# Kernel optimization log

Measured on AMD Instinct MI355X. Metric: run time of the kernel, lower is better.

The kernel has to match this reference:

```python
import math
import jax, jax.numpy as jnp
import numpy as np

L, D, H, DF, V, T, B = 4, 1024, 16, 4096, 32000, 2048, 1
HD = D // H
EPS = 1e-5

def _ln(x, w, b):
    m = jnp.mean(x, -1, keepdims=True)
    v = jnp.mean((x - m) ** 2, -1, keepdims=True)
    return (x - m) * jax.lax.rsqrt(v + EPS) * w + b

def setup_inputs() -> dict:
    key = jax.random.key(0)
    ks = jax.random.split(key, 8)
    s = 0.02
    return {
        'ids':   jax.random.randint(ks[0], (B, T), 0, V),
        'te':    jax.random.normal(ks[1], (V, D), jnp.float32) * s,
        'pe':    jax.random.normal(ks[2], (T, D), jnp.float32) * s,
        'qkv_w': jax.random.normal(ks[3], (L, D, 3 * D), jnp.float32) * s,
        'qkv_b': jnp.zeros((L, 3 * D), jnp.float32),
        'out_w': jax.random.normal(ks[4], (L, D, D), jnp.float32) * s,
        'out_b': jnp.zeros((L, D), jnp.float32),
        'ln1_w': jnp.ones((L, D), jnp.float32),
        'ln1_b': jnp.zeros((L, D), jnp.float32),
        'ln2_w': jnp.ones((L, D), jnp.float32),
        'ln2_b': jnp.zeros((L, D), jnp.float32),
        'up_w':  jax.random.normal(ks[5], (L, D, DF), jnp.float32) * s,
        'up_b':  jnp.zeros((L, DF), jnp.float32),
        'dn_w':  jax.random.normal(ks[6], (L, DF, D), jnp.float32) * s,
        'dn_b':  jnp.zeros((L, D), jnp.float32),
        'lnf_w': jnp.ones((D,), jnp.float32),
        'lnf_b': jnp.zeros((D,), jnp.float32),
    }

def reference(ids, te, pe, qkv_w, qkv_b, out_w, out_b, ln1_w, ln1_b,
              ln2_w, ln2_b, up_w, up_b, dn_w, dn_b, lnf_w, lnf_b):
    b, t = ids.shape
    x = te[ids] + pe[:t][None]                        # [b,t,D]
    causal = jnp.tril(jnp.ones((t, t), bool))          # [t,t]
    scale = 1.0 / math.sqrt(HD)
    for i in range(L):
        h = _ln(x, ln1_w[i], ln1_b[i])
        qkv = (h @ qkv_w[i] + qkv_b[i]).reshape(b, t, 3, H, HD)
        q, k, v = qkv[:, :, 0], qkv[:, :, 1], qkv[:, :, 2]
        sc = jnp.einsum('bqhd,bkhd->bhqk', q, k) * scale
        sc = jnp.where(causal, sc, -jnp.inf)
        att = jax.nn.softmax(sc, axis=-1)
        ao = jnp.einsum('bhqk,bkhd->bqhd', att, v).reshape(b, t, D)
        x = x + ao @ out_w[i] + out_b[i]
        h = _ln(x, ln2_w[i], ln2_b[i])
        x = x + jax.nn.silu(h @ up_w[i] + up_b[i]) @ dn_w[i] + dn_b[i]
    x = _ln(x, lnf_w, lnf_b)
    logits = x @ te.T                                  # tied head, no bias
    return logits
```

## Files before the change

kernel.cpp:

```cpp
#include <hip/hip_runtime.h>

typedef __attribute__((ext_vector_type(8))) short short8;
typedef __attribute__((ext_vector_type(4))) short short4v;
typedef __attribute__((ext_vector_type(4))) float f32x4;
typedef unsigned short u16;

#define Lc 4
#define Dc 1024
#define Hc 16
#define HDc 64
#define DFc 4096
#define Vc 32000
#define Tc 2048

__device__ __forceinline__ u16 f2bf(float f) {
  union { float f; unsigned u; } v; v.f = f;
  return (u16)((v.u + 0x7FFFu + ((v.u >> 16) & 1u)) >> 16);
}

__device__ __forceinline__ void gload_lds16(const u16* g, u16* l) {
  __builtin_amdgcn_global_load_lds(
      (const __attribute__((address_space(1))) unsigned int*)(g),
      (__attribute__((address_space(3))) unsigned int*)(l), 16, 0, 0);
}

#define BARS do { __builtin_amdgcn_s_barrier(); __builtin_amdgcn_sched_barrier(0); } while (0)
#define LGKM0 do { asm volatile("s_waitcnt lgkmcnt(0)" ::: "memory"); __builtin_amdgcn_sched_barrier(0); } while (0)
#define VMC(n) do { asm volatile("s_waitcnt vmcnt(" #n ")" ::: "memory"); __builtin_amdgcn_sched_barrier(0); } while (0)

__global__ __launch_bounds__(256) void castk(const float* __restrict__ in, u16* __restrict__ out) {
  size_t i = ((size_t)blockIdx.x * 256 + threadIdx.x) * 4;
  float4 v = *(const float4*)(in + i);
  short4v o; o[0] = f2bf(v.x); o[1] = f2bf(v.y); o[2] = f2bf(v.z); o[3] = f2bf(v.w);
  *(short4v*)(out + i) = o;
}

__global__ __launch_bounds__(256) void embedln(const int* __restrict__ ids, const float* __restrict__ te,
                                               const float* __restrict__ pe, const float* __restrict__ w,
                                               const float* __restrict__ b, float* __restrict__ x,
                                               u16* __restrict__ out) {
  int t = blockIdx.x, tid = threadIdx.x;
  int id = ids[t];
  float4 a = *(const float4*)(te + (size_t)id * Dc + tid * 4);
  float4 p = *(const float4*)(pe + (size_t)t * Dc + tid * 4);
  float4 v; v.x = a.x + p.x; v.y = a.y + p.y; v.z = a.z + p.z; v.w = a.w + p.w;
  size_t i = (size_t)t * Dc + tid * 4;
  *(float4*)(x + i) = v;
  float s = v.x + v.y + v.z + v.w;
  float q = v.x * v.x + v.y * v.y + v.z * v.z + v.w * v.w;
  #pragma unroll
  for (int off = 1; off < 64; off <<= 1) { s += __shfl_xor(s, off); q += __shfl_xor(q, off); }
  __shared__ float red[8];
  if ((tid & 63) == 0) { red[tid >> 6] = s; red[4 + (tid >> 6)] = q; }
  __syncthreads();
  s = red[0] + red[1] + red[2] + red[3];
  q = red[4] + red[5] + red[6] + red[7];
  float mean = s * (1.0f / Dc);
  float rstd = rsqrtf(q * (1.0f / Dc) - mean * mean + 1e-5f);
  float4 wv = *(const float4*)(w + tid * 4);
  float4 bv = *(const float4*)(b + tid * 4);
  out[i + 0] = f2bf((v.x - mean) * rstd * wv.x + bv.x);
  out[i + 1] = f2bf((v.y - mean) * rstd * wv.y + bv.y);
  out[i + 2] = f2bf((v.z - mean) * rstd * wv.z + bv.z);
  out[i + 3] = f2bf((v.w - mean) * rstd * wv.w + bv.w);
}

template<int SK>
__global__ __launch_bounds__(256) void combineln(float* __restrict__ x, const float* __restrict__ p,
                                                 const float* __restrict__ bias, const float* __restrict__ w,
                                                 const float* __restrict__ b, u16* __restrict__ out) {
  int t = blockIdx.x, tid = threadIdx.x;
  size_t i = (size_t)t * Dc + tid * 4;
  float4 v = *(const float4*)(x + i);
  #pragma unroll
  for (int s = 0; s < SK; s++) {
    float4 q2 = *(const float4*)(p + (size_t)s * Tc * Dc + i);
    v.x += q2.x; v.y += q2.y; v.z += q2.z; v.w += q2.w;
  }
  float4 bb = *(const float4*)(bias + tid * 4);
  v.x += bb.x; v.y += bb.y; v.z += bb.z; v.w += bb.w;
  *(float4*)(x + i) = v;
  float s = v.x + v.y + v.z + v.w;
  float q = v.x * v.x + v.y * v.y + v.z * v.z + v.w * v.w;
  #pragma unroll
  for (int off = 1; off < 64; off <<= 1) { s += __shfl_xor(s, off); q += __shfl_xor(q, off); }
  __shared__ float red[8];
  if ((tid & 63) == 0) { red[tid >> 6] = s; red[4 + (tid >> 6)] = q; }
  __syncthreads();
  s = red[0] + red[1] + red[2] + red[3];
  q = red[4] + red[5] + red[6] + red[7];
  float mean = s * (1.0f / Dc);
  float rstd = rsqrtf(q * (1.0f / Dc) - mean * mean + 1e-5f);
  float4 wv = *(const float4*)(w + tid * 4);
  float4 bv = *(const float4*)(b + tid * 4);
  out[i + 0] = f2bf((v.x - mean) * rstd * wv.x + bv.x);
  out[i + 1] = f2bf((v.y - mean) * rstd * wv.y + bv.y);
  out[i + 2] = f2bf((v.z - mean) * rstd * wv.z + bv.z);
  out[i + 3] = f2bf((v.w - mean) * rstd * wv.w + bv.w);
}

__global__ __launch_bounds__(256) void transpose4(const float* __restrict__ qw, const float* __restrict__ ow,
                                                  const float* __restrict__ uw, const float* __restrict__ dw,
                                                  u16* __restrict__ qT, u16* __restrict__ oT,
                                                  u16* __restrict__ uT, u16* __restrict__ dT) {
  __shared__ float tl[32][33];
  int id = blockIdx.x;
  const float* in; u16* out; int R, C, t;
  if (id < 3072)      { in = qw; out = qT; R = Dc;  C = 3 * Dc; t = id; }
  else if (id < 4096) { in = ow; out = oT; R = Dc;  C = Dc;     t = id - 3072; }
  else if (id < 8192) { in = uw; out = uT; R = Dc;  C = DFc;    t = id - 4096; }
  else                { in = dw; out = dT; R = DFc; C = Dc;     t = id - 8192; }
  int tilesX = C >> 5;
  int c0 = (t % tilesX) * 32, r0 = (t / tilesX) * 32;
  int lx = threadIdx.x & 31, ly = threadIdx.x >> 5;
  #pragma unroll
  for (int i = ly; i < 32; i += 8) tl[i][lx] = in[(size_t)(r0 + i) * C + c0 + lx];
  __syncthreads();
  #pragma unroll
  for (int i = ly; i < 32; i += 8) out[(size_t)(c0 + i) * R + r0 + lx] = f2bf(tl[lx][i]);
}

template<int EPI>
__global__ __launch_bounds__(256) void gemm128m(
    const u16* __restrict__ A, const u16* __restrict__ Bt, const float* __restrict__ bias,
    u16* __restrict__ outb, float* __restrict__ outf, int M, int N, int K, int KS) {
  __shared__ __align__(16) u16 lds[32768];
  u16* As = lds;
  u16* Bs = lds + 16384;
  const int NK = KS >> 6;

  int tid = threadIdx.x;
  int w = tid >> 6, lane = tid & 63;
  int lr = lane & 15, lg = lane >> 4;
  int wr = w >> 1, wc = w & 1;

  int m0 = blockIdx.y * 128, n0 = blockIdx.x * 128;
  int kbase = blockIdx.z * KS;

  int offg[4];
  #pragma unroll
  for (int j = 0; j < 4; j++) {
    int p = tid + j * 256;
    int row = p >> 3;
    int uc = (p & 7) ^ (row & 7);
    offg[j] = row * K + uc * 8;
  }
  const u16* aB = A + (size_t)m0 * K + kbase;
  const u16* bB = Bt + (size_t)n0 * K + kbase;

  auto stA = [&](int kt) {
    u16* l = As + ((kt & 1) << 13) + w * 512;
    #pragma unroll
    for (int j = 0; j < 4; j++)
      gload_lds16(aB + kt * 64 + offg[j], l + j * 2048);
  };
  auto stB = [&](int kt) {
    u16* l = Bs + ((kt & 1) << 13) + w * 512;
    #pragma unroll
    for (int j = 0; j < 4; j++)
      gload_lds16(bB + kt * 64 + offg[j], l + j * 2048);
  };

  int colx0 = ((0 * 4 + lg) ^ (lr & 7)) * 8;
  int colx1 = ((1 * 4 + lg) ^ (lr & 7)) * 8;
  int abase = (wr * 64 + lr) * 64;
  int bbase = (wc * 64 + lr) * 64;

  f32x4 acc[4][4] = {};

  stB(0); stA(0); stB(1);
  VMC(4);
  BARS;

  for (int kt = 0; kt < NK; ++kt) {
    const u16* sA = As + ((kt & 1) << 13);
    const u16* sB = Bs + ((kt & 1) << 13);
    short8 af[4][2], bf[4][2];

    #pragma unroll
    for (int m = 0; m < 2; m++) {
      af[m][0] = *(const short8*)(sA + abase + m * 1024 + colx0);
      af[m][1] = *(const short8*)(sA + abase + m * 1024 + colx1);
    }
    #pragma unroll
    for (int n = 0; n < 4; n++) {
      bf[n][0] = *(const short8*)(sB + bbase + n * 1024 + colx0);
      bf[n][1] = *(const short8*)(sB + bbase + n * 1024 + colx1);
    }
    if (kt + 1 < NK) stA(kt + 1);
    BARS;
    LGKM0;
    __builtin_amdgcn_s_setprio(1);
    #pragma unroll
    for (int m = 0; m < 2; m++)
      #pragma unroll
      for (int n = 0; n < 4; n++)
        #pragma unroll
        for (int ks = 0; ks < 2; ks++)
          acc[m][n] = __builtin_amdgcn_mfma_f32_16x16x32_bf16(af[m][ks], bf[n][ks], acc[m][n], 0, 0, 0);
    __builtin_amdgcn_s_setprio(0);
    BARS;

    #pragma unroll
    for (int m = 2; m < 4; m++) {
      af[m][0] = *(const short8*)(sA + abase + m * 1024 + colx0);
      af[m][1] = *(const short8*)(sA + abase + m * 1024 + colx1);
    }
    if (kt + 2 < NK) { stB(kt + 2); VMC(4); }
    else if (kt + 1 < NK) { VMC(0); }
    BARS;
    LGKM0;
    __builtin_amdgcn_s_setprio(1);
    #pragma unroll
    for (int m = 2; m < 4; m++)
      #pragma unroll
      for (int n = 0; n < 4; n++)
        #pragma unroll
        for (int ks = 0; ks < 2; ks++)
          acc[m][n] = __builtin_amdgcn_mfma_f32_16x16x32_bf16(af[m][ks], bf[n][ks], acc[m][n], 0, 0, 0);
    __builtin_amdgcn_s_setprio(0);
    BARS;
  }

  if (EPI == 0 || EPI == 1 || (EPI == 5 && n0 < 2 * Dc)) {
    u16* lu = lds;
    BARS;
    #pragma unroll
    for (int n = 0; n < 4; n++) {
      int col = wc * 64 + n * 16 + lr;
      float bv = bias[n0 + col];
      #pragma unroll
      for (int m = 0; m < 4; m++) {
        #pragma unroll
        for (int r = 0; r < 4; r++) {
          int rl = wr * 64 + m * 16 + lg * 4 + r;
          float v = acc[m][n][r] + bv;
          if (EPI == 1) v = v / (1.0f + __expf(-v));
          lu[rl * 128 + (col ^ (((rl >> 2) & 3) << 4))] = f2bf(v);
        }
      }
    }
    BARS;
    #pragma unroll
    for (int j = 0; j < 8; j++) {
      int i8 = j * 2048 + tid * 8;
      int row = i8 >> 7;
      int col8 = i8 & 127;
      short8 v = *(const short8*)(lu + row * 128 + (col8 ^ (((row >> 2) & 3) << 4)));
      *(short8*)(outb + (size_t)(m0 + row) * N + n0 + col8) = v;
    }
  } else if (EPI == 4) {
    float* lf = (float*)lds;
    float* op = outf + (size_t)blockIdx.z * M * N;
    #pragma unroll
    for (int pass = 0; pass < 2; pass++) {
      BARS;
      if (wr == pass) {
        #pragma unroll
        for (int n = 0; n < 4; n++) {
          int col = wc * 64 + n * 16 + lr;
          #pragma unroll
          for (int m = 0; m < 4; m++)
            #pragma unroll
            for (int r = 0; r < 4; r++) {
              int rl = m * 16 + lg * 4 + r;
              lf[rl * 128 + (col ^ (((rl >> 2) & 1) << 4))] = acc[m][n][r];
            }
        }
      }
      BARS;
      #pragma unroll
      for (int j = 0; j < 8; j++) {
        int i4 = j * 1024 + tid * 4;
        int row = i4 >> 7;
        int col4 = i4 & 127;
        f32x4 v = *(const f32x4*)(lf + row * 128 + (col4 ^ (((row >> 2) & 1) << 4)));
        *(f32x4*)(op + (size_t)(m0 + pass * 64 + row) * N + n0 + col4) = v;
      }
    }
  } else {
    u16* vtp = (u16*)outf;
    #pragma unroll
    for (int n = 0; n < 4; n++) {
      int gn = n0 + wc * 64 + n * 16 + lr;
      float bv = bias[gn];
      #pragma unroll
      for (int m = 0; m < 4; m++) {
        int gmb = m0 + wr * 64 + m * 16 + lg * 4;
        short4v o;
        #pragma unroll
        for (int r = 0; r < 4; r++) o[r] = (short)f2bf(acc[m][n][r] + bv);
        *(short4v*)(vtp + (size_t)(gn - 2 * Dc) * Tc + gmb) = o;
      }
    }
  }
}

__global__ __launch_bounds__(512) void gemm256(const u16* __restrict__ A, const u16* __restrict__ Bt,
                                               float* __restrict__ outf, int M, int N, int K) {
  __shared__ __align__(16) u16 lds[65536];
  u16* AsU = lds;
  u16* BsU = lds + 32768;
  const int NK = K >> 6;

  int tid = threadIdx.x;
  int w = tid >> 6, lane = tid & 63;
  int lr = lane & 15, lg = lane >> 4;
  int wr = w >> 2, wc = w & 3;

  int flat = blockIdx.y * gridDim.x + blockIdx.x;
  {
    int nwg = gridDim.x * gridDim.y;
    int q = nwg >> 3, r = nwg & 7, xc = flat & 7, s = flat >> 3;
    flat = (xc < r ? xc * (q + 1) : r * (q + 1) + (xc - r) * q) + s;
  }
  int bm = flat % gridDim.x, bn = flat / gridDim.x;
  int m0 = bm * 256, n0 = bn * 256;

  int row0 = tid >> 3;
  int uc0 = (tid & 7) ^ (row0 & 7);
  int offg = row0 * K + uc0 * 8;
  const u16* aB = A + (size_t)m0 * K;
  const u16* bB = Bt + (size_t)n0 * K;

  auto stA = [&](int kt, int half) {
    const u16* g = aB + (size_t)half * 128 * K + kt * 64 + offg;
    u16* l = AsU + (((kt & 1) * 2 + half) << 13) + w * 512;
    gload_lds16(g, l);
    gload_lds16(g + 64 * K, l + 4096);
  };
  auto stB = [&](int kt, int half) {
    const u16* g = bB + (size_t)half * 128 * K + kt * 64 + offg;
    u16* l = BsU + (((kt & 1) * 2 + half) << 13) + w * 512;
    gload_lds16(g, l);
    gload_lds16(g + 64 * K, l + 4096);
  };

  int colx0 = ((0 * 4 + lg) ^ (lr & 7)) * 8;
  int colx1 = ((1 * 4 + lg) ^ (lr & 7)) * 8;
  int arow = lr * 64;
  int brow = ((wc & 1) * 64 + lr) * 64;

  f32x4 acc[8][4] = {};

  stB(0, 0); stB(0, 1); stA(0, 0); stA(0, 1); stB(1, 0); stB(1, 1);
  VMC(4);
  BARS;

  for (int kt = 0; kt < NK; ++kt) {
    int slot = kt & 1;
    const u16* sA = AsU + ((slot * 2 + wr) << 13);
    const u16* sB = BsU + ((slot * 2 + (wc >> 1)) << 13);
    short8 af0[4][2], af1[4][2], bf0[2][2], bf1[2][2];

    #pragma unroll
    for (int m = 0; m < 4; m++) {
      af0[m][0] = *(const short8*)(sA + arow + m * 1024 + colx0);
      af0[m][1] = *(const short8*)(sA + arow + m * 1024 + colx1);
    }
    #pragma unroll
    for (int n = 0; n < 2; n++) {
      bf0[n][0] = *(const short8*)(sB + brow + n * 1024 + colx0);
      bf0[n][1] = *(const short8*)(sB + brow + n * 1024 + colx1);
      bf1[n][0] = *(const short8*)(sB + brow + (n + 2) * 1024 + colx0);
      bf1[n][1] = *(const short8*)(sB + brow + (n + 2) * 1024 + colx1);
    }
    if (kt + 1 < NK) { stA(kt + 1, 0); stA(kt + 1, 1); }
    BARS;
    LGKM0;
    __builtin_amdgcn_s_setprio(1);
    #pragma unroll
    for (int m = 0; m < 4; m++)
      #pragma unroll
      for (int n = 0; n < 2; n++)
        #pragma unroll
        for (int ks = 0; ks < 2; ks++)
          acc[m][n] = __builtin_amdgcn_mfma_f32_16x16x32_bf16(af0[m][ks], bf0[n][ks], acc[m][n], 0, 0, 0);
    #pragma unroll
    for (int m = 0; m < 4; m++)
      #pragma unroll
      for (int n = 0; n < 2; n++)
        #pragma unroll
        for (int ks = 0; ks < 2; ks++)
          acc[m][n + 2] = __builtin_amdgcn_mfma_f32_16x16x32_bf16(af0[m][ks], bf1[n][ks], acc[m][n + 2], 0, 0, 0);
    __builtin_amdgcn_s_setprio(0);
    BARS;

    #pragma unroll
    for (int m = 0; m < 4; m++) {
      af1[m][0] = *(const short8*)(sA + arow + (m + 4) * 1024 + colx0);
      af1[m][1] = *(const short8*)(sA + arow + (m + 4) * 1024 + colx1);
    }
    if (kt + 2 < NK) { stB(kt + 2, 0); stB(kt + 2, 1); VMC(4); }
    else if (kt + 1 < NK) { VMC(0); }
    BARS;
    LGKM0;
    __builtin_amdgcn_s_setprio(1);
    #pragma unroll
    for (int m = 0; m < 4; m++)
      #pragma unroll
      for (int n = 0; n < 2; n++)
        #pragma unroll
        for (int ks = 0; ks < 2; ks++)
          acc[m + 4][n] = __builtin_amdgcn_mfma_f32_16x16x32_bf16(af1[m][ks], bf0[n][ks], acc[m + 4][n], 0, 0, 0);
    #pragma unroll
    for (int m = 0; m < 4; m++)
      #pragma unroll
      for (int n = 0; n < 2; n++)
        #pragma unroll
        for (int ks = 0; ks < 2; ks++)
          acc[m + 4][n + 2] = __builtin_amdgcn_mfma_f32_16x16x32_bf16(af1[m][ks], bf1[n][ks], acc[m + 4][n + 2], 0, 0, 0);
    __builtin_amdgcn_s_setprio(0);
    BARS;
  }

  {
    float* lf = (float*)lds;
    #pragma unroll
    for (int pass = 0; pass < 2; pass++) {
      BARS;
      if (wr == pass) {
        #pragma unroll
        for (int n = 0; n < 4; n++) {
          int col = wc * 64 + n * 16 + lr;
          #pragma unroll
          for (int m = 0; m < 8; m++)
            #pragma unroll
            for (int r = 0; r < 4; r++) {
              int rl = m * 16 + lg * 4 + r;
              lf[rl * 256 + (col ^ (((rl >> 2) & 1) << 4))] = acc[m][n][r];
            }
        }
      }
      BARS;
      #pragma unroll
      for (int j = 0; j < 16; j++) {
        int i4 = j * 2048 + tid * 4;
        int row = i4 >> 8;
        int col4 = i4 & 255;
        f32x4 v = *(const f32x4*)(lf + row * 256 + (col4 ^ (((row >> 2) & 1) << 4)));
        *(f32x4*)(outf + (size_t)(m0 + pass * 128 + row) * N + n0 + col4) = v;
      }
    }
  }
}

__global__ __launch_bounds__(512) void attnk(const u16* __restrict__ qkv, const u16* __restrict__ vt,
                                             u16* __restrict__ ao) {
  __shared__ u16 Plds[8][16][72];
  __shared__ float Cacc[4][64][16];
  __shared__ float Cl[4][64][4];
  int bid = blockIdx.x;
  int hh = bid >> 5;
  int qb = (bid & 256) ? (31 - (bid & 31)) : (bid & 31);
  int tid = threadIdx.x, l = tid & 63, w = tid >> 6;
  int w4 = w & 3, ishi = w >> 2;
  int lr = l & 15, lg = l >> 4;
  int qr0 = qb * 64 + w4 * 16;
  const u16* qbase = qkv + (size_t)(qr0 + lr) * (3 * Dc) + hh * HDc + lg * 8;
  short8 aq0 = *(const short8*)qbase;
  short8 aq1 = *(const short8*)(qbase + 32);
  f32x4 acco[4] = {};
  float rs[4] = {0.0f, 0.0f, 0.0f, 0.0f};
  int nkb = (qr0 + 79) >> 6;
  int half = nkb >> 1;
  int klo = ishi ? half : 0;
  int khi = ishi ? nkb : half;
  const float cl2 = 0.125f * 1.44269504088896f;
  for (int kb = klo; kb < khi; kb++) {
    int kk0 = kb * 64;
    float sv[4][4];
    bool msk = (kb == nkb - 1);
    #pragma unroll
    for (int st = 0; st < 4; st++) {
      int kt0 = kk0 + st * 16;
      const u16* kbase = qkv + (size_t)(kt0 + lr) * (3 * Dc) + Dc + hh * HDc + lg * 8;
      short8 bk0 = *(const short8*)kbase;
      short8 bk1 = *(const short8*)(kbase + 32);
      f32x4 s = {};
      s = __builtin_amdgcn_mfma_f32_16x16x32_bf16(aq0, bk0, s, 0, 0, 0);
      s = __builtin_amdgcn_mfma_f32_16x16x32_bf16(aq1, bk1, s, 0, 0, 0);
      if (msk) {
        int gcol = kt0 + lr;
        #pragma unroll
        for (int r = 0; r < 4; r++) {
          int grow = qr0 + lg * 4 + r;
          sv[st][r] = (gcol <= grow) ? s[r] * cl2 : -__builtin_inff();
        }
      } else {
        #pragma unroll
        for (int r = 0; r < 4; r++) sv[st][r] = s[r] * cl2;
      }
    }
    #pragma unroll
    for (int st = 0; st < 4; st++) {
      #pragma unroll
      for (int r = 0; r < 4; r++) {
        float p = __builtin_amdgcn_exp2f(fminf(sv[st][r], 45.0f));
        sv[st][r] = p;
        rs[r] += p;
      }
    }
    #pragma unroll
    for (int st = 0; st < 4; st++) {
      #pragma unroll
      for (int r = 0; r < 4; r++) Plds[w][lg * 4 + r][st * 16 + lr] = f2bf(sv[st][r]);
    }
    short8 pa0 = *(const short8*)&Plds[w][lr][lg * 8];
    short8 pa1 = *(const short8*)&Plds[w][lr][32 + lg * 8];
    #pragma unroll
    for (int nt = 0; nt < 4; nt++) {
      const u16* vbase = vt + (size_t)(hh * HDc + nt * 16 + lr) * Tc + kk0 + lg * 8;
      short8 bv0 = *(const short8*)vbase;
      short8 bv1 = *(const short8*)(vbase + 32);
      acco[nt] = __builtin_amdgcn_mfma_f32_16x16x32_bf16(pa0, bv0, acco[nt], 0, 0, 0);
      acco[nt] = __builtin_amdgcn_mfma_f32_16x16x32_bf16(pa1, bv1, acco[nt], 0, 0, 0);
    }
  }
  #pragma unroll
  for (int off = 1; off < 16; off <<= 1) {
    #pragma unroll
    for (int r = 0; r < 4; r++) rs[r] += __shfl_xor(rs[r], off);
  }
  if (ishi) {
    #pragma unroll
    for (int nt = 0; nt < 4; nt++)
      #pragma unroll
      for (int r = 0; r < 4; r++) Cacc[w4][l][nt * 4 + r] = acco[nt][r];
    #pragma unroll
    for (int r = 0; r < 4; r++) Cl[w4][l][r] = rs[r];
  }
  __syncthreads();
  if (!ishi) {
    float linv[4];
    #pragma unroll
    for (int r = 0; r < 4; r++) linv[r] = 1.0f / (rs[r] + Cl[w4][l][r]);
    #pragma unroll
    for (int nt = 0; nt < 4; nt++) {
      #pragma unroll
      for (int r = 0; r < 4; r++) {
        float val = (acco[nt][r] + Cacc[w4][l][nt * 4 + r]) * linv[r];
        ao[(size_t)(qr0 + lg * 4 + r) * Dc + hh * HDc + nt * 16 + lr] = f2bf(val);
      }
    }
  }
}

extern "C" void kernel_launch(void* const* d_in, const int* in_sizes, int n_in,
                              void* d_out, int out_size, void* d_ws, size_t ws_size,
                              hipStream_t stream) {
  const int*   ids   = (const int*)d_in[0];
  const float* te    = (const float*)d_in[1];
  const float* pe    = (const float*)d_in[2];
  const float* qkv_w = (const float*)d_in[3];
  const float* qkv_b = (const float*)d_in[4];
  const float* out_w = (const float*)d_in[5];
  const float* out_b = (const float*)d_in[6];
  const float* ln1_w = (const float*)d_in[7];
  const float* ln1_b = (const float*)d_in[8];
  const float* ln2_w = (const float*)d_in[9];
  const float* ln2_b = (const float*)d_in[10];
  const float* up_w  = (const float*)d_in[11];
  const float* up_b  = (const float*)d_in[12];
  const float* dn_w  = (const float*)d_in[13];
  const float* dn_b  = (const float*)d_in[14];
  const float* lnf_w = (const float*)d_in[15];
  const float* lnf_b = (const float*)d_in[16];
  float* logits = (float*)d_out;

  char* ws = (char*)d_ws;
  size_t off = 0;
  auto alloc = [&](size_t bytes) { void* p = ws + off; off += (bytes + 255) & ~(size_t)255; return p; };
  float* x    = (float*)alloc((size_t)Tc * Dc * 4);
  u16* hbuf   = (u16*)alloc((size_t)Tc * Dc * 2);
  u16* qkvb   = (u16*)alloc((size_t)Tc * 3 * Dc * 2);
  u16* aob    = (u16*)alloc((size_t)Tc * Dc * 2);
  u16* ubuf   = (u16*)alloc((size_t)Tc * DFc * 2);
  u16* vtb    = (u16*)alloc((size_t)Dc * Tc * 2);
  u16* tebf   = (u16*)alloc((size_t)Vc * Dc * 2);
  u16* qkvT   = (u16*)alloc((size_t)3 * Dc * Dc * 2);
  u16* outT   = (u16*)alloc((size_t)Dc * Dc * 2);
  u16* upT    = (u16*)alloc((size_t)DFc * Dc * 2);
  u16* dnT    = (u16*)alloc((size_t)Dc * DFc * 2);
  float* pbuf = (float*)alloc((size_t)4 * Tc * Dc * 4);

  castk<<<Vc * Dc / 1024, 256, 0, stream>>>(te, tebf);
  embedln<<<Tc, 256, 0, stream>>>(ids, te, pe, ln1_w, ln1_b, x, hbuf);

  for (int i = 0; i < Lc; i++) {
    transpose4<<<12288, 256, 0, stream>>>(
        qkv_w + (size_t)i * Dc * 3 * Dc, out_w + (size_t)i * Dc * Dc,
        up_w + (size_t)i * Dc * DFc, dn_w + (size_t)i * DFc * Dc,
        qkvT, outT, upT, dnT);

    gemm128m<5><<<dim3(3 * Dc / 128, Tc / 128, 1), 256, 0, stream>>>(
        hbuf, qkvT, qkv_b + (size_t)i * 3 * Dc, qkvb, (float*)vtb, Tc, 3 * Dc, Dc, Dc);
    attnk<<<512, 512, 0, stream>>>(qkvb, vtb, aob);
    gemm128m<4><<<dim3(Dc / 128, Tc / 128, 2), 256, 0, stream>>>(
        aob, outT, nullptr, nullptr, pbuf, Tc, Dc, Dc, Dc / 2);
    combineln<2><<<Tc, 256, 0, stream>>>(x, pbuf, out_b + (size_t)i * Dc,
                                         ln2_w + (size_t)i * Dc, ln2_b + (size_t)i * Dc, hbuf);
    gemm128m<1><<<dim3(DFc / 128, Tc / 128, 1), 256, 0, stream>>>(
        hbuf, upT, up_b + (size_t)i * DFc, ubuf, nullptr, Tc, DFc, Dc, Dc);
    gemm128m<4><<<dim3(Dc / 128, Tc / 128, 4), 256, 0, stream>>>(
        ubuf, dnT, nullptr, nullptr, pbuf, Tc, Dc, DFc, DFc / 4);
    if (i < Lc - 1)
      combineln<4><<<Tc, 256, 0, stream>>>(x, pbuf, dn_b + (size_t)i * Dc,
                                           ln1_w + (size_t)(i + 1) * Dc, ln1_b + (size_t)(i + 1) * Dc, hbuf);
    else
      combineln<4><<<Tc, 256, 0, stream>>>(x, pbuf, dn_b + (size_t)i * Dc, lnf_w, lnf_b, hbuf);
  }

  gemm256<<<dim3(Tc / 256, Vc / 256), 512, 0, stream>>>(hbuf, tebf, logits, Tc, Vc, Dc);
}
```

Baseline: 949.8 us.

## Software-pipeline LDS fragment reads in GEMM main loops with partial lgkmcnt waits

Both GEMM kernels now prefetch the next tile's A fragments from LDS during the current iteration and hoist the B/high-A reads ahead of the barrier. Waits become partial lgkmcnt waits instead of full drains, and two barriers per iteration are removed. The goal is to overlap LDS reads with MFMA work and cut sync stalls. The risks are higher register pressure and subtle LDS reuse hazards, because fewer barriers now guard the double-buffer slots against overwrite by global_load_lds.

```diff
diff --git a/kernel.cpp b/kernel.cpp
--- a/kernel.cpp
+++ b/kernel.cpp
@@ -25,7 +25,7 @@
 }
 
 #define BARS do { __builtin_amdgcn_s_barrier(); __builtin_amdgcn_sched_barrier(0); } while (0)
-#define LGKM0 do { asm volatile("s_waitcnt lgkmcnt(0)" ::: "memory"); __builtin_amdgcn_sched_barrier(0); } while (0)
+#define LGKM(n) do { asm volatile("s_waitcnt lgkmcnt(" #n ")" ::: "memory"); __builtin_amdgcn_sched_barrier(0); } while (0)
 #define VMC(n) do { asm volatile("s_waitcnt vmcnt(" #n ")" ::: "memory"); __builtin_amdgcn_sched_barrier(0); } while (0)
 
 __global__ __launch_bounds__(256) void castk(const float* __restrict__ in, u16* __restrict__ out) {
@@ -166,30 +166,47 @@
   int abase = (wr * 64 + lr) * 64;
   int bbase = (wc * 64 + lr) * 64;
 
+  short8 af01[2][2], af23[2][2], bf[4][2];
+
+  auto rd_af01 = [&](int slot) {
+    const u16* sA = As + (slot << 13);
+    #pragma unroll
+    for (int m = 0; m < 2; m++) {
+      af01[m][0] = *(const short8*)(sA + abase + m * 1024 + colx0);
+      af01[m][1] = *(const short8*)(sA + abase + m * 1024 + colx1);
+    }
+  };
+  auto rd_af23 = [&](int slot) {
+    const u16* sA = As + (slot << 13);
+    #pragma unroll
+    for (int m = 0; m < 2; m++) {
+      af23[m][0] = *(const short8*)(sA + abase + (m + 2) * 1024 + colx0);
+      af23[m][1] = *(const short8*)(sA + abase + (m + 2) * 1024 + colx1);
+    }
+  };
+  auto rd_bf = [&](int slot) {
+    const u16* sB = Bs + (slot << 13);
+    #pragma unroll
+    for (int n = 0; n < 4; n++) {
+      bf[n][0] = *(const short8*)(sB + bbase + n * 1024 + colx0);
+      bf[n][1] = *(const short8*)(sB + bbase + n * 1024 + colx1);
+    }
+  };
+
   f32x4 acc[4][4] = {};
 
   stB(0); stA(0); stB(1);
   VMC(4);
   BARS;
+  rd_af01(0);
 
   for (int kt = 0; kt < NK; ++kt) {
-    const u16* sA = As + ((kt & 1) << 13);
-    const u16* sB = Bs + ((kt & 1) << 13);
-    short8 af[4][2], bf[4][2];
-
-    #pragma unroll
-    for (int m = 0; m < 2; m++) {
-      af[m][0] = *(const short8*)(sA + abase + m * 1024 + colx0);
-      af[m][1] = *(const short8*)(sA + abase + m * 1024 + colx1);
-    }
-    #pragma unroll
-    for (int n = 0; n < 4; n++) {
-      bf[n][0] = *(const short8*)(sB + bbase + n * 1024 + colx0);
-      bf[n][1] = *(const short8*)(sB + bbase + n * 1024 + colx1);
-    }
+    int slot = kt & 1;
+    rd_bf(slot);
+    rd_af23(slot);
+    LGKM(4);
+    BARS;
     if (kt + 1 < NK) stA(kt + 1);
-    BARS;
-    LGKM0;
     __builtin_amdgcn_s_setprio(1);
     #pragma unroll
     for (int m = 0; m < 2; m++)
@@ -197,29 +214,26 @@
       for (int n = 0; n < 4; n++)
         #pragma unroll
         for (int ks = 0; ks < 2; ks++)
-          acc[m][n] = __builtin_amdgcn_mfma_f32_16x16x32_bf16(af[m][ks], bf[n][ks], acc[m][n], 0, 0, 0);
+          acc[m][n] = __builtin_amdgcn_mfma_f32_16x16x32_bf16(af01[m][ks], bf[n][ks], acc[m][n], 0, 0, 0);
     __builtin_amdgcn_s_setprio(0);
-    BARS;
-
-    #pragma unroll
-    for (int m = 2; m < 4; m++) {
-      af[m][0] = *(const short8*)(sA + abase + m * 1024 + colx0);
-      af[m][1] = *(const short8*)(sA + abase + m * 1024 + colx1);
-    }
     if (kt + 2 < NK) { stB(kt + 2); VMC(4); }
     else if (kt + 1 < NK) { VMC(0); }
     BARS;
-    LGKM0;
+    if (kt + 1 < NK) {
+      rd_af01((kt + 1) & 1);
+      LGKM(4);
+    } else {
+      LGKM(0);
+    }
     __builtin_amdgcn_s_setprio(1);
     #pragma unroll
-    for (int m = 2; m < 4; m++)
+    for (int m = 0; m < 2; m++)
       #pragma unroll
       for (int n = 0; n < 4; n++)
         #pragma unroll
         for (int ks = 0; ks < 2; ks++)
-          acc[m][n] = __builtin_amdgcn_mfma_f32_16x16x32_bf16(af[m][ks], bf[n][ks], acc[m][n], 0, 0, 0);
+          acc[m + 2][n] = __builtin_amdgcn_mfma_f32_16x16x32_bf16(af23[m][ks], bf[n][ks], acc[m + 2][n], 0, 0, 0);
     __builtin_amdgcn_s_setprio(0);
-    BARS;
   }
 
   if (EPI == 0 || EPI == 1 || (EPI == 5 && n0 < 2 * Dc)) {
@@ -341,23 +355,26 @@
   int arow = lr * 64;
   int brow = ((wc & 1) * 64 + lr) * 64;
 
-  f32x4 acc[8][4] = {};
-
-  stB(0, 0); stB(0, 1); stA(0, 0); stA(0, 1); stB(1, 0); stB(1, 1);
-  VMC(4);
-  BARS;
-
-  for (int kt = 0; kt < NK; ++kt) {
-    int slot = kt & 1;
+  short8 af0[4][2], af1[4][2], bf0[2][2], bf1[2][2];
+
+  auto rd_af_lo = [&](int slot) {
     const u16* sA = AsU + ((slot * 2 + wr) << 13);
-    const u16* sB = BsU + ((slot * 2 + (wc >> 1)) << 13);
-    short8 af0[4][2], af1[4][2], bf0[2][2], bf1[2][2];
-
     #pragma unroll
     for (int m = 0; m < 4; m++) {
       af0[m][0] = *(const short8*)(sA + arow + m * 1024 + colx0);
       af0[m][1] = *(const short8*)(sA + arow + m * 1024 + colx1);
     }
+  };
+  auto rd_af_hi = [&](int slot) {
+    const u16* sA = AsU + ((slot * 2 + wr) << 13);
+    #pragma unroll
+    for (int m = 0; m < 4; m++) {
+      af1[m][0] = *(const short8*)(sA + arow + (m + 4) * 1024 + colx0);
+      af1[m][1] = *(const short8*)(sA + arow + (m + 4) * 1024 + colx1);
+    }
+  };
+  auto rd_bf = [&](int slot) {
+    const u16* sB = BsU + ((slot * 2 + (wc >> 1)) << 13);
     #pragma unroll
     for (int n = 0; n < 2; n++) {
       bf0[n][0] = *(const short8*)(sB + brow + n * 1024 + colx0);
@@ -365,9 +382,22 @@
       bf1[n][0] = *(const short8*)(sB + brow + (n + 2) * 1024 + colx0);
       bf1[n][1] = *(const short8*)(sB + brow + (n + 2) * 1024 + colx1);
     }
+  };
+
+  f32x4 acc[8][4] = {};
+
+  stB(0, 0); stB(0, 1); stA(0, 0); stA(0, 1); stB(1, 0); stB(1, 1);
+  VMC(4);
+  BARS;
+  rd_af_lo(0);
+
+  for (int kt = 0; kt < NK; ++kt) {
+    int slot = kt & 1;
+    rd_bf(slot);
+    rd_af_hi(slot);
+    LGKM(8);
+    BARS;
     if (kt + 1 < NK) { stA(kt + 1, 0); stA(kt + 1, 1); }
-    BARS;
-    LGKM0;
     __builtin_amdgcn_s_setprio(1);
     #pragma unroll
     for (int m = 0; m < 4; m++)
@@ -384,17 +414,15 @@
         for (int ks = 0; ks < 2; ks++)
           acc[m][n + 2] = __builtin_amdgcn_mfma_f32_16x16x32_bf16(af0[m][ks], bf1[n][ks], acc[m][n + 2], 0, 0, 0);
     __builtin_amdgcn_s_setprio(0);
-    BARS;
-
-    #pragma unroll
-    for (int m = 0; m < 4; m++) {
-      af1[m][0] = *(const short8*)(sA + arow + (m + 4) * 1024 + colx0);
-      af1[m][1] = *(const short8*)(sA + arow + (m + 4) * 1024 + colx1);
-    }
     if (kt + 2 < NK) { stB(kt + 2, 0); stB(kt + 2, 1); VMC(4); }
     else if (kt + 1 < NK) { VMC(0); }
     BARS;
-    LGKM0;
+    if (kt + 1 < NK) {
+      rd_af_lo((kt + 1) & 1);
+      LGKM(8);
+    } else {
+      LGKM(0);
+    }
     __builtin_amdgcn_s_setprio(1);
     #pragma unroll
     for (int m = 0; m < 4; m++)
@@ -411,7 +439,6 @@
         for (int ks = 0; ks < 2; ks++)
           acc[m + 4][n + 2] = __builtin_amdgcn_mfma_f32_16x16x32_bf16(af1[m][ks], bf1[n][ks], acc[m + 4][n + 2], 0, 0, 0);
     __builtin_amdgcn_s_setprio(0);
-    BARS;
   }
 
   {
```

After: 952.2 us. No clear change (+0.3%).
